# Performance work log

Hardware: AMD Instinct MI355X
Metric: run time of the kernel (lower is better)

The kernel has to match this reference:

```python
import jax, jax.numpy as jnp
import numpy as np
import math

D_MODEL = 1024
N_HEADS = 16
D_KV = 64
NUM_BUCKETS = 32
MAX_DISTANCE = 128
BATCH = 4
SEQ = 2048


def _relative_position_bucket(relative_position, num_buckets=NUM_BUCKETS, max_distance=MAX_DISTANCE):
    # bidirectional=True (encoder)
    num_buckets //= 2
    relative_buckets = (relative_position > 0).astype(jnp.int32) * num_buckets
    rp = jnp.abs(relative_position)
    max_exact = num_buckets // 2
    is_small = rp < max_exact
    rp_safe = jnp.maximum(rp, 1)  # avoid log(0); masked by is_small anyway
    rp_if_large = max_exact + (
        jnp.log(rp_safe.astype(jnp.float32) / max_exact)
        / math.log(max_distance / max_exact)
        * (num_buckets - max_exact)
    ).astype(jnp.int32)
    rp_if_large = jnp.minimum(rp_if_large, num_buckets - 1)
    relative_buckets += jnp.where(is_small, rp, rp_if_large)
    return relative_buckets


def compute_bias(rel_bias, q_len, k_len):
    context = jnp.arange(q_len)[:, None]
    memory = jnp.arange(k_len)[None, :]
    buckets = _relative_position_bucket(memory - context)  # [q, k]
    values = rel_bias[buckets]                              # [q, k, h]
    return jnp.transpose(values, (2, 0, 1))[None]           # [1, h, q, k]


def setup_inputs() -> dict:
    key = jax.random.key(0)
    ks = jax.random.split(key, 6)
    s = 1.0 / math.sqrt(D_MODEL)
    return {
        "hidden_states": jax.random.normal(ks[0], (BATCH, SEQ, D_MODEL), jnp.float32),
        "wq": jax.random.normal(ks[1], (D_MODEL, N_HEADS * D_KV), jnp.float32) * s,
        "wk": jax.random.normal(ks[2], (D_MODEL, N_HEADS * D_KV), jnp.float32) * s,
        "wv": jax.random.normal(ks[3], (D_MODEL, N_HEADS * D_KV), jnp.float32) * s,
        "wo": jax.random.normal(ks[4], (N_HEADS * D_KV, D_MODEL), jnp.float32) * s,
        "rel_bias": jax.random.normal(ks[5], (NUM_BUCKETS, N_HEADS), jnp.float32) * 0.5,
    }


def reference(hidden_states, wq, wk, wv, wo, rel_bias):
    B, S, _ = hidden_states.shape

    def shape(x):  # [B,S,H*Dk] -> [B,H,S,Dk]
        return x.reshape(B, S, N_HEADS, D_KV).transpose(0, 2, 1, 3)

    q = shape(hidden_states @ wq)
    k = shape(hidden_states @ wk)
    v = shape(hidden_states @ wv)

    # NOTE: T5 does NOT scale by 1/sqrt(d_kv)
    scores = jnp.einsum("bhqd,bhkd->bhqk", q, k)
    position_bias = compute_bias(rel_bias, S, S)  # [1,H,S,S]
    scores = scores + position_bias
    attn = jax.nn.softmax(scores.astype(jnp.float32), axis=-1).astype(scores.dtype)
    ctx = jnp.einsum("bhqk,bhkd->bhqd", attn, v)
    ctx = ctx.transpose(0, 2, 1, 3).reshape(B, S, N_HEADS * D_KV)
    return ctx @ wo
```

## Files before the change

kernel.cpp:

```cpp
#include <hip/hip_runtime.h>
#include <hip/hip_bf16.h>

typedef unsigned short u16;
typedef unsigned int   u32;
typedef __bf16 bf16x8 __attribute__((ext_vector_type(8)));
typedef float  f32x4  __attribute__((ext_vector_type(4)));
typedef u16    u16x8  __attribute__((ext_vector_type(8)));
typedef u16    u16x4  __attribute__((ext_vector_type(4)));

#define MFMA16(a,b,c) __builtin_amdgcn_mfma_f32_16x16x32_bf16(a,b,c,0,0,0)
#define LOG2E 1.4426950408889634f

__device__ __forceinline__ u16 f2b(float f) {
    u32 u = __builtin_bit_cast(u32, f);
    u32 r = (u + 0x7FFFu + ((u >> 16) & 1u)) >> 16;
    return (u16)r;
}

typedef const __attribute__((address_space(1))) u32* gaddr_t;
typedef __attribute__((address_space(3))) u32*       laddr_t;
__device__ __forceinline__ void gl_lds16(const void* g, void* l) {
    __builtin_amdgcn_global_load_lds((gaddr_t)g, (laddr_t)l, 16, 0, 0);
}

__global__ __launch_bounds__(256) void prep_kernel(
        const float* __restrict__ H, const float* __restrict__ wq,
        const float* __restrict__ wk, const float* __restrict__ wv,
        const float* __restrict__ wo, const float* __restrict__ rel_bias,
        u16* __restrict__ Hb, u16* __restrict__ Wt, u16* __restrict__ Wot,
        float* __restrict__ tab) {
    __shared__ u16 tile[64 * 72];
    int bi = blockIdx.x;
    int t = threadIdx.x;
    if (bi < 4096) {
        int i = (bi * 256 + t) * 8;
        float4 a = *(const float4*)(H + i);
        float4 b = *(const float4*)(H + i + 4);
        u16x8 o = { f2b(a.x), f2b(a.y), f2b(a.z), f2b(a.w),
                    f2b(b.x), f2b(b.y), f2b(b.z), f2b(b.w) };
        *(u16x8*)(Hb + i) = o;
    } else if (bi < 5120) {
        int g2 = bi - 4096;
        int g = g2 >> 8, rem = g2 & 255;
        int n0 = (rem >> 4) * 64, k0 = (rem & 15) * 64;
        const float* src = (g == 0) ? wq : (g == 1) ? wk : (g == 2) ? wv : wo;
        u16* dst = (g < 3) ? (Wt + g * 1048576) : Wot;
#pragma unroll
        for (int rr = 0; rr < 4; ++rr) {
            int idx = rr * 256 + t;
            int kr = idx >> 4, c = idx & 15;
            float4 v = *(const float4*)(src + (k0 + kr) * 1024 + n0 + c * 4);
            u16x4 o = { f2b(v.x), f2b(v.y), f2b(v.z), f2b(v.w) };
            *(u16x4*)&tile[kr * 72 + c * 4] = o;
        }
        __syncthreads();
#pragma unroll
        for (int rr = 0; rr < 2; ++rr) {
            int idx = rr * 256 + t;
            int n = idx >> 3, c = idx & 7;
            u16x8 o;
#pragma unroll
            for (int j = 0; j < 8; ++j) o[j] = tile[(c * 8 + j) * 72 + n];
            *(u16x8*)(dst + (n0 + n) * 1024 + k0 + c * 8) = o;
        }
    } else {
        int i = (bi - 5120) * 256 + t;
        int h = i >> 12;
        int idx = i & 4095;
        int delta = idx - 2048;
        int bucket = (delta > 0) ? 16 : 0;
        int rp = delta < 0 ? -delta : delta;
        if (rp < 8) {
            bucket += rp;
        } else {
            double v = log((double)rp / 8.0) / log(16.0) * 8.0;
            int tt = (int)v;
            int b2 = 8 + tt;
            bucket += (b2 < 15) ? b2 : 15;
        }
        tab[h * 4096 + idx] = rel_bias[bucket * 16 + h] * LOG2E;
    }
}

template <int MODE>
__global__ __launch_bounds__(256) void gemm_bt(
        const u16* __restrict__ A, const u16* __restrict__ Bt, int K, int N,
        u16* __restrict__ q_out, u16* __restrict__ k_out, u16* __restrict__ v_out,
        float* __restrict__ f_out) {
    __shared__ u16 As[128 * 32];
    __shared__ u16 Bs[128 * 32];
    __shared__ u16 vt_tile[MODE == 0 ? 128 * 136 : 1];
    int t = threadIdx.x;
    int lane = t & 63, w = t >> 6;
    int wm = w & 1, wn = w >> 1;
    int ln = lane & 15, quad = lane >> 4;
    int m0 = blockIdx.x * 128, n0 = blockIdx.y * 128;
    const u16* Ab = A + m0 * K;
    const u16* Bb = Bt + n0 * K;
    f32x4 acc[4][4] = {};
    int nk = K >> 5;
    for (int kt = 0; kt < nk; ++kt) {
        int k0 = kt * 32;
#pragma unroll
        for (int rr = 0; rr < 2; ++rr) {
            int idx = rr * 256 + t;
            int row = idx >> 2, c = (idx & 3) ^ (row & 3);
            gl_lds16(Ab + row * K + k0 + c * 8, ((char*)As) + idx * 16);
            gl_lds16(Bb + row * K + k0 + c * 8, ((char*)Bs) + idx * 16);
        }
        __syncthreads();
        bf16x8 af[4], bfr[4];
#pragma unroll
        for (int mb = 0; mb < 4; ++mb) {
            int row = wm * 64 + mb * 16 + ln;
            af[mb] = *(const bf16x8*)&As[row * 32 + ((quad ^ (row & 3)) << 3)];
        }
#pragma unroll
        for (int nb = 0; nb < 4; ++nb) {
            int row = wn * 64 + nb * 16 + ln;
            bfr[nb] = *(const bf16x8*)&Bs[row * 32 + ((quad ^ (row & 3)) << 3)];
        }
#pragma unroll
        for (int mb = 0; mb < 4; ++mb)
#pragma unroll
            for (int nb = 0; nb < 4; ++nb)
                acc[mb][nb] = MFMA16(af[mb], bfr[nb], acc[mb][nb]);
        __syncthreads();
    }
    if (MODE == 0 && n0 >= 2048) {
#pragma unroll
        for (int mb = 0; mb < 4; ++mb)
#pragma unroll
            for (int nb = 0; nb < 4; ++nb)
#pragma unroll
                for (int r = 0; r < 4; ++r) {
                    int np = wn * 64 + nb * 16 + ln;
                    int mp = wm * 64 + mb * 16 + quad * 4 + r;
                    vt_tile[np * 136 + mp] = f2b(acc[mb][nb][r]);
                }
        __syncthreads();
        int h0 = (n0 >> 6) & 15;
        int b = m0 >> 11;
        int s0 = m0 & 2047;
#pragma unroll
        for (int j = 0; j < 8; ++j) {
            int e = j * 256 + t;
            int d_all = e >> 4;
            int sc = e & 15;
            int hh = h0 + (d_all >> 6);
            int d = d_all & 63;
            u16x8 val = *(const u16x8*)&vt_tile[d_all * 136 + sc * 8];
            *(u16x8*)(v_out + (b * 16 + hh) * 131072 + d * 2048 + s0 + sc * 8) = val;
        }
    } else {
#pragma unroll
        for (int mb = 0; mb < 4; ++mb)
#pragma unroll
            for (int nb = 0; nb < 4; ++nb)
#pragma unroll
                for (int r = 0; r < 4; ++r) {
                    int m = m0 + wm * 64 + mb * 16 + quad * 4 + r;
                    int n = n0 + wn * 64 + nb * 16 + ln;
                    float v = acc[mb][nb][r];
                    if (MODE == 0) {
                        int which = n >> 10, h = (n >> 6) & 15, d = n & 63;
                        int b = m >> 11, s = m & 2047;
                        u16* dst = (which == 0) ? q_out : k_out;
                        float scale = (which == 0) ? LOG2E : 1.0f;
                        dst[(((b << 4) + h) * 2048 + s) * 64 + d] = f2b(v * scale);
                    } else {
                        f_out[m * N + n] = v;
                    }
                }
    }
}

__global__ __launch_bounds__(256, 3) void attn_kernel(
        const u16* __restrict__ Qb, const u16* __restrict__ Kb,
        const u16* __restrict__ Vt, const float* __restrict__ bias_tab,
        u16* __restrict__ ctx) {
    __shared__ u16 Ks[2][64 * 64];
    __shared__ u16 Vs[2][64 * 64];
    __shared__ u16 Ps[4][16 * 64];
    __shared__ float sb[384];
    int t = threadIdx.x;
    int lane = t & 63, w = t >> 6;
    int ln = lane & 15, quad = lane >> 4;
    int bh = blockIdx.x >> 5;
    int qtile = blockIdx.x & 31;
    int h = bh & 15, b = bh >> 4;
    int q0 = qtile * 64;

    float chi = bias_tab[h * 4096 + 2048 + 1500];
    float clo = bias_tab[h * 4096 + 2048 - 1500];

    const float* tb = bias_tab + h * 4096 + 1857;
    for (int i = t; i < 384; i += 256) sb[i] = tb[i];

    int qa = q0 + w * 16 + ln;
    const u16* qptr = Qb + (bh * 2048 + qa) * 64 + quad * 8;
    bf16x8 qf0 = *(const bf16x8*)(qptr);
    bf16x8 qf1 = *(const bf16x8*)(qptr + 32);

    const u16* Kbase = Kb + bh * 2048 * 64;
    const u16* Vbase = Vt + bh * 64 * 2048;

    f32x4 oacc[4] = {};
    float l_i = 0.0f;
    int cb2_base = 191 - w * 16 + quad * 4 - ln;
    int swl = ln & 7;

    auto stage = [&](int kb, int bufidx) {
#pragma unroll
        for (int it = 0; it < 2; ++it) {
            int idx = it * 256 + t;
            int row = idx >> 3, c = (idx & 7) ^ (row & 7);
            gl_lds16(Kbase + (kb + row) * 64 + c * 8,
                     ((char*)&Ks[bufidx][0]) + idx * 16);
            gl_lds16(Vbase + row * 2048 + kb + c * 8,
                     ((char*)&Vs[bufidx][0]) + idx * 16);
        }
    };

    auto compute = [&](int kb0, const u16* Kc, const u16* Vc) {
        f32x4 sacc[4];
        int diff = kb0 - q0;
        if (diff >= 192 || diff <= -192) {
            float c0 = (diff > 0) ? chi : clo;
            f32x4 ci = {c0, c0, c0, c0};
            __builtin_amdgcn_s_setprio(1);
#pragma unroll
            for (int nb = 0; nb < 4; ++nb) {
                int key = nb * 16 + ln;
                int sw = key & 7;
                bf16x8 kf0 = *(const bf16x8*)&Kc[key * 64 + ((quad ^ sw) << 3)];
                bf16x8 kf1 = *(const bf16x8*)&Kc[key * 64 + (((quad ^ 4) ^ sw) << 3)];
                f32x4 scc = MFMA16(kf0, qf0, ci);
                sacc[nb] = MFMA16(kf1, qf1, scc);
            }
            __builtin_amdgcn_s_setprio(0);
        } else {
            int cb = diff + cb2_base;
            __builtin_amdgcn_s_setprio(1);
#pragma unroll
            for (int nb = 0; nb < 4; ++nb) {
                int key = nb * 16 + ln;
                int sw = key & 7;
                const float* bp = &sb[cb + nb * 16];
                f32x4 ci = {bp[0], bp[1], bp[2], bp[3]};
                bf16x8 kf0 = *(const bf16x8*)&Kc[key * 64 + ((quad ^ sw) << 3)];
                bf16x8 kf1 = *(const bf16x8*)&Kc[key * 64 + (((quad ^ 4) ^ sw) << 3)];
                f32x4 scc = MFMA16(kf0, qf0, ci);
                sacc[nb] = MFMA16(kf1, qf1, scc);
            }
            __builtin_amdgcn_s_setprio(0);
        }

        float p[4][4];
        float ls0 = 0.f, ls1 = 0.f, ls2 = 0.f, ls3 = 0.f;
#pragma unroll
        for (int nb = 0; nb < 4; ++nb) {
            float e0 = __builtin_amdgcn_exp2f(sacc[nb][0]);
            float e1 = __builtin_amdgcn_exp2f(sacc[nb][1]);
            float e2 = __builtin_amdgcn_exp2f(sacc[nb][2]);
            float e3 = __builtin_amdgcn_exp2f(sacc[nb][3]);
            p[nb][0] = e0; p[nb][1] = e1; p[nb][2] = e2; p[nb][3] = e3;
            ls0 += e0; ls1 += e1; ls2 += e2; ls3 += e3;
        }
        l_i += (ls0 + ls1) + (ls2 + ls3);

        u16* pw = &Ps[w][0];
#pragma unroll
        for (int nb = 0; nb < 4; ++nb) {
            u32 lo, hi;
            asm("v_cvt_pk_bf16_f32 %0, %1, %2" : "=v"(lo) : "v"(p[nb][0]), "v"(p[nb][1]));
            asm("v_cvt_pk_bf16_f32 %0, %1, %2" : "=v"(hi) : "v"(p[nb][2]), "v"(p[nb][3]));
            int c = nb * 2 + (quad >> 1);
            u32* dst = (u32*)&pw[ln * 64 + ((c ^ swl) << 3) + (quad & 1) * 4];
            dst[0] = lo;
            dst[1] = hi;
        }

#pragma unroll
        for (int kc = 0; kc < 2; ++kc) {
            bf16x8 pf = *(const bf16x8*)&pw[ln * 64 + (((kc * 4 + quad) ^ swl) << 3)];
            __builtin_amdgcn_s_setprio(1);
#pragma unroll
            for (int nb = 0; nb < 4; ++nb) {
                int d = nb * 16 + ln;
                int vc = (kc * 4 + quad) ^ (d & 7);
                bf16x8 vf = *(const bf16x8*)&Vc[d * 64 + (vc << 3)];
                oacc[nb] = MFMA16(pf, vf, oacc[nb]);
            }
            __builtin_amdgcn_s_setprio(0);
        }
    };

    stage(0, 0);
    for (int kt = 0; kt < 31; ++kt) {
        int cur = kt & 1;
        stage((kt + 1) * 64, cur ^ 1);
        asm volatile("s_waitcnt vmcnt(4)" ::: "memory");
        __builtin_amdgcn_sched_barrier(0);
        __builtin_amdgcn_s_barrier();
        compute(kt * 64, &Ks[cur][0], &Vs[cur][0]);
        __builtin_amdgcn_s_barrier();
    }
    asm volatile("s_waitcnt vmcnt(0)" ::: "memory");
    __builtin_amdgcn_sched_barrier(0);
    __builtin_amdgcn_s_barrier();
    compute(31 * 64, &Ks[1][0], &Vs[1][0]);

    l_i += __shfl_xor(l_i, 16);
    l_i += __shfl_xor(l_i, 32);
    float linv = 1.0f / l_i;
#pragma unroll
    for (int r = 0; r < 4; ++r) {
        float lr = __shfl(linv, quad * 4 + r);
        int q = q0 + w * 16 + quad * 4 + r;
#pragma unroll
        for (int nb = 0; nb < 4; ++nb)
            ctx[(b * 2048 + q) * 1024 + h * 64 + nb * 16 + ln] = f2b(oacc[nb][r] * lr);
    }
}

extern "C" void kernel_launch(void* const* d_in, const int* in_sizes, int n_in,
                              void* d_out, int out_size, void* d_ws, size_t ws_size,
                              hipStream_t stream) {
    const float* H   = (const float*)d_in[0];
    const float* wq  = (const float*)d_in[1];
    const float* wk  = (const float*)d_in[2];
    const float* wv  = (const float*)d_in[3];
    const float* wo  = (const float*)d_in[4];
    const float* rel = (const float*)d_in[5];
    float* out = (float*)d_out;

    char* ws = (char*)d_ws;
    u16* Hb    = (u16*)(ws);
    u16* Wt    = (u16*)(ws + 16777216);
    u16* Wot   = (u16*)(ws + 23068672);
    u16* Qb    = (u16*)(ws + 25165824);
    u16* Kb    = (u16*)(ws + 41943040);
    u16* Vt    = (u16*)(ws + 58720256);
    float* bias_tab = (float*)(ws + 75497472);
    u16* ctx = Hb;

    prep_kernel<<<5376, 256, 0, stream>>>(H, wq, wk, wv, wo, rel, Hb, Wt, Wot, bias_tab);
    gemm_bt<0><<<dim3(64, 24), 256, 0, stream>>>(Hb, Wt, 1024, 3072, Qb, Kb, Vt, nullptr);
    attn_kernel<<<2048, 256, 0, stream>>>(Qb, Kb, Vt, bias_tab, ctx);
    gemm_bt<1><<<dim3(64, 8), 256, 0, stream>>>(ctx, Wot, 1024, 1024, nullptr, nullptr, nullptr, out);
}
```

Before: 307.0 us.

## Process two query tiles per attention block and keep P in registers

Each attention block now handles 128 queries (two 64-row groups) against each staged K/V tile, halving the number of blocks and the K/V global-to-LDS staging traffic per query. The P·V product is computed with 16x16x16 MFMAs and V as the A operand, so the exponentiated probabilities stay in registers instead of being written to and read back from LDS. Block-to-(head,qtile) mapping is swizzled, occupancy hint is raised to 4, and output stores are vectorized. It raises register pressure and uses the smaller-K MFMA, which issues twice as many PV instructions.

```diff
diff --git a/kernel.cpp b/kernel.cpp
--- a/kernel.cpp
+++ b/kernel.cpp
@@ -4,12 +4,28 @@
 typedef unsigned short u16;
 typedef unsigned int   u32;
 typedef __bf16 bf16x8 __attribute__((ext_vector_type(8)));
+typedef __bf16 bf16x4 __attribute__((ext_vector_type(4)));
+typedef short  s16x4  __attribute__((ext_vector_type(4)));
 typedef float  f32x4  __attribute__((ext_vector_type(4)));
 typedef u16    u16x8  __attribute__((ext_vector_type(8)));
 typedef u16    u16x4  __attribute__((ext_vector_type(4)));
+typedef u32    u32x2  __attribute__((ext_vector_type(2)));
 
 #define MFMA16(a,b,c) __builtin_amdgcn_mfma_f32_16x16x32_bf16(a,b,c,0,0,0)
 #define LOG2E 1.4426950408889634f
+
+__device__ __forceinline__ f32x4 mfma16k16(bf16x4 a, bf16x4 b, f32x4 c) {
+#if __has_builtin(__builtin_amdgcn_mfma_f32_16x16x16bf16_1k)
+    return __builtin_amdgcn_mfma_f32_16x16x16bf16_1k(
+        __builtin_bit_cast(s16x4, a), __builtin_bit_cast(s16x4, b), c, 0, 0, 0);
+#elif __has_builtin(__builtin_amdgcn_mfma_f32_16x16x16_bf16_1k)
+    return __builtin_amdgcn_mfma_f32_16x16x16_bf16_1k(
+        __builtin_bit_cast(s16x4, a), __builtin_bit_cast(s16x4, b), c, 0, 0, 0);
+#else
+    asm("v_mfma_f32_16x16x16_bf16 %0, %1, %2, %0" : "+v"(c) : "v"(a), "v"(b));
+    return c;
+#endif
+}
 
 __device__ __forceinline__ u16 f2b(float f) {
     u32 u = __builtin_bit_cast(u32, f);
@@ -175,21 +191,21 @@
     }
 }
 
-__global__ __launch_bounds__(256, 3) void attn_kernel(
+__global__ __launch_bounds__(256, 4) void attn_kernel(
         const u16* __restrict__ Qb, const u16* __restrict__ Kb,
         const u16* __restrict__ Vt, const float* __restrict__ bias_tab,
         u16* __restrict__ ctx) {
     __shared__ u16 Ks[2][64 * 64];
     __shared__ u16 Vs[2][64 * 64];
-    __shared__ u16 Ps[4][16 * 64];
     __shared__ float sb[384];
     int t = threadIdx.x;
     int lane = t & 63, w = t >> 6;
     int ln = lane & 15, quad = lane >> 4;
-    int bh = blockIdx.x >> 5;
-    int qtile = blockIdx.x & 31;
+    int bid = blockIdx.x;
+    int bh = (bid & 7) * 8 + (bid >> 7);
+    int qtile = (bid >> 3) & 15;
     int h = bh & 15, b = bh >> 4;
-    int q0 = qtile * 64;
+    int q0 = qtile * 128;
 
     float chi = bias_tab[h * 4096 + 2048 + 1500];
     float clo = bias_tab[h * 4096 + 2048 - 1500];
@@ -197,18 +213,19 @@
     const float* tb = bias_tab + h * 4096 + 1857;
     for (int i = t; i < 384; i += 256) sb[i] = tb[i];
 
-    int qa = q0 + w * 16 + ln;
-    const u16* qptr = Qb + (bh * 2048 + qa) * 64 + quad * 8;
-    bf16x8 qf0 = *(const bf16x8*)(qptr);
-    bf16x8 qf1 = *(const bf16x8*)(qptr + 32);
+    const u16* qbase = Qb + (bh * 2048 + q0 + w * 16 + ln) * 64 + quad * 8;
+    bf16x8 qf[2][2];
+    qf[0][0] = *(const bf16x8*)(qbase);
+    qf[0][1] = *(const bf16x8*)(qbase + 32);
+    qf[1][0] = *(const bf16x8*)(qbase + 64 * 64);
+    qf[1][1] = *(const bf16x8*)(qbase + 64 * 64 + 32);
 
     const u16* Kbase = Kb + bh * 2048 * 64;
     const u16* Vbase = Vt + bh * 64 * 2048;
 
-    f32x4 oacc[4] = {};
-    float l_i = 0.0f;
+    f32x4 oacc[2][4] = {};
+    float l0 = 0.0f, l1 = 0.0f;
     int cb2_base = 191 - w * 16 + quad * 4 - ln;
-    int swl = ln & 7;
 
     auto stage = [&](int kb, int bufidx) {
 #pragma unroll
@@ -223,80 +240,74 @@
     };
 
     auto compute = [&](int kb0, const u16* Kc, const u16* Vc) {
-        f32x4 sacc[4];
-        int diff = kb0 - q0;
-        if (diff >= 192 || diff <= -192) {
-            float c0 = (diff > 0) ? chi : clo;
-            f32x4 ci = {c0, c0, c0, c0};
-            __builtin_amdgcn_s_setprio(1);
+        f32x4 sacc[2][4];
+        int diffs[2] = {kb0 - q0, kb0 - q0 - 64};
+        __builtin_amdgcn_s_setprio(1);
+#pragma unroll
+        for (int nb = 0; nb < 4; ++nb) {
+            int key = nb * 16 + ln;
+            int sw = key & 7;
+            bf16x8 kf0 = *(const bf16x8*)&Kc[key * 64 + ((quad ^ sw) << 3)];
+            bf16x8 kf1 = *(const bf16x8*)&Kc[key * 64 + (((quad ^ 4) ^ sw) << 3)];
+#pragma unroll
+            for (int g = 0; g < 2; ++g) {
+                int diff = diffs[g];
+                f32x4 ci;
+                if (diff >= 192 || diff <= -192) {
+                    float c0 = (diff > 0) ? chi : clo;
+                    ci = {c0, c0, c0, c0};
+                } else {
+                    const float* bp = &sb[diff + cb2_base + nb * 16];
+                    ci = {bp[0], bp[1], bp[2], bp[3]};
+                }
+                f32x4 scc = MFMA16(kf0, qf[g][0], ci);
+                sacc[g][nb] = MFMA16(kf1, qf[g][1], scc);
+            }
+        }
+        __builtin_amdgcn_s_setprio(0);
+
+        bf16x4 pb[2][4];
+#pragma unroll
+        for (int g = 0; g < 2; ++g) {
+            float s0 = 0.f, s1 = 0.f, s2 = 0.f, s3 = 0.f;
 #pragma unroll
             for (int nb = 0; nb < 4; ++nb) {
-                int key = nb * 16 + ln;
-                int sw = key & 7;
-                bf16x8 kf0 = *(const bf16x8*)&Kc[key * 64 + ((quad ^ sw) << 3)];
-                bf16x8 kf1 = *(const bf16x8*)&Kc[key * 64 + (((quad ^ 4) ^ sw) << 3)];
-                f32x4 scc = MFMA16(kf0, qf0, ci);
-                sacc[nb] = MFMA16(kf1, qf1, scc);
+                float e0 = __builtin_amdgcn_exp2f(sacc[g][nb][0]);
+                float e1 = __builtin_amdgcn_exp2f(sacc[g][nb][1]);
+                float e2 = __builtin_amdgcn_exp2f(sacc[g][nb][2]);
+                float e3 = __builtin_amdgcn_exp2f(sacc[g][nb][3]);
+                s0 += e0; s1 += e1; s2 += e2; s3 += e3;
+                u32 lo, hi;
+                asm("v_cvt_pk_bf16_f32 %0, %1, %2" : "=v"(lo) : "v"(e0), "v"(e1));
+                asm("v_cvt_pk_bf16_f32 %0, %1, %2" : "=v"(hi) : "v"(e2), "v"(e3));
+                u32x2 uv = {lo, hi};
+                pb[g][nb] = __builtin_bit_cast(bf16x4, uv);
             }
-            __builtin_amdgcn_s_setprio(0);
-        } else {
-            int cb = diff + cb2_base;
-            __builtin_amdgcn_s_setprio(1);
-#pragma unroll
-            for (int nb = 0; nb < 4; ++nb) {
-                int key = nb * 16 + ln;
-                int sw = key & 7;
-                const float* bp = &sb[cb + nb * 16];
-                f32x4 ci = {bp[0], bp[1], bp[2], bp[3]};
-                bf16x8 kf0 = *(const bf16x8*)&Kc[key * 64 + ((quad ^ sw) << 3)];
-                bf16x8 kf1 = *(const bf16x8*)&Kc[key * 64 + (((quad ^ 4) ^ sw) << 3)];
-                f32x4 scc = MFMA16(kf0, qf0, ci);
-                sacc[nb] = MFMA16(kf1, qf1, scc);
+            if (g == 0) l0 += (s0 + s1) + (s2 + s3);
+            else        l1 += (s0 + s1) + (s2 + s3);
+        }
+
+        __builtin_amdgcn_s_setprio(1);
+#pragma unroll
+        for (int kc = 0; kc < 4; ++kc) {
+            bf16x4 vA[4];
+#pragma unroll
+            for (int nd = 0; nd < 4; ++nd) {
+                int d = nd * 16 + ln;
+                int ch = (kc * 2 + (quad >> 1)) ^ (d & 7);
+                vA[nd] = *(const bf16x4*)&Vc[d * 64 + (ch << 3) + ((quad & 1) << 2)];
             }
-            __builtin_amdgcn_s_setprio(0);
-        }
-
-        float p[4][4];
-        float ls0 = 0.f, ls1 = 0.f, ls2 = 0.f, ls3 = 0.f;
-#pragma unroll
-        for (int nb = 0; nb < 4; ++nb) {
-            float e0 = __builtin_amdgcn_exp2f(sacc[nb][0]);
-            float e1 = __builtin_amdgcn_exp2f(sacc[nb][1]);
-            float e2 = __builtin_amdgcn_exp2f(sacc[nb][2]);
-            float e3 = __builtin_amdgcn_exp2f(sacc[nb][3]);
-            p[nb][0] = e0; p[nb][1] = e1; p[nb][2] = e2; p[nb][3] = e3;
-            ls0 += e0; ls1 += e1; ls2 += e2; ls3 += e3;
-        }
-        l_i += (ls0 + ls1) + (ls2 + ls3);
-
-        u16* pw = &Ps[w][0];
-#pragma unroll
-        for (int nb = 0; nb < 4; ++nb) {
-            u32 lo, hi;
-            asm("v_cvt_pk_bf16_f32 %0, %1, %2" : "=v"(lo) : "v"(p[nb][0]), "v"(p[nb][1]));
-            asm("v_cvt_pk_bf16_f32 %0, %1, %2" : "=v"(hi) : "v"(p[nb][2]), "v"(p[nb][3]));
-            int c = nb * 2 + (quad >> 1);
-            u32* dst = (u32*)&pw[ln * 64 + ((c ^ swl) << 3) + (quad & 1) * 4];
-            dst[0] = lo;
-            dst[1] = hi;
-        }
-
-#pragma unroll
-        for (int kc = 0; kc < 2; ++kc) {
-            bf16x8 pf = *(const bf16x8*)&pw[ln * 64 + (((kc * 4 + quad) ^ swl) << 3)];
-            __builtin_amdgcn_s_setprio(1);
-#pragma unroll
-            for (int nb = 0; nb < 4; ++nb) {
-                int d = nb * 16 + ln;
-                int vc = (kc * 4 + quad) ^ (d & 7);
-                bf16x8 vf = *(const bf16x8*)&Vc[d * 64 + (vc << 3)];
-                oacc[nb] = MFMA16(pf, vf, oacc[nb]);
-            }
-            __builtin_amdgcn_s_setprio(0);
-        }
+#pragma unroll
+            for (int nd = 0; nd < 4; ++nd)
+#pragma unroll
+                for (int g = 0; g < 2; ++g)
+                    oacc[g][nd] = mfma16k16(vA[nd], pb[g][kc], oacc[g][nd]);
+        }
+        __builtin_amdgcn_s_setprio(0);
     };
 
     stage(0, 0);
+    asm volatile("s_waitcnt lgkmcnt(0)" ::: "memory");
     for (int kt = 0; kt < 31; ++kt) {
         int cur = kt & 1;
         stage((kt + 1) * 64, cur ^ 1);
@@ -311,16 +322,19 @@
     __builtin_amdgcn_s_barrier();
     compute(31 * 64, &Ks[1][0], &Vs[1][0]);
 
-    l_i += __shfl_xor(l_i, 16);
-    l_i += __shfl_xor(l_i, 32);
-    float linv = 1.0f / l_i;
-#pragma unroll
-    for (int r = 0; r < 4; ++r) {
-        float lr = __shfl(linv, quad * 4 + r);
-        int q = q0 + w * 16 + quad * 4 + r;
-#pragma unroll
-        for (int nb = 0; nb < 4; ++nb)
-            ctx[(b * 2048 + q) * 1024 + h * 64 + nb * 16 + ln] = f2b(oacc[nb][r] * lr);
+    l0 += __shfl_xor(l0, 16); l0 += __shfl_xor(l0, 32);
+    l1 += __shfl_xor(l1, 16); l1 += __shfl_xor(l1, 32);
+    float linv[2] = {1.0f / l0, 1.0f / l1};
+#pragma unroll
+    for (int g = 0; g < 2; ++g) {
+        int q = q0 + g * 64 + w * 16 + ln;
+        u16* cp = ctx + (b * 2048 + q) * 1024 + h * 64 + quad * 4;
+#pragma unroll
+        for (int nd = 0; nd < 4; ++nd) {
+            u16x4 o = { f2b(oacc[g][nd][0] * linv[g]), f2b(oacc[g][nd][1] * linv[g]),
+                        f2b(oacc[g][nd][2] * linv[g]), f2b(oacc[g][nd][3] * linv[g]) };
+            *(u16x4*)(cp + nd * 16) = o;
+        }
     }
 }
 
@@ -347,6 +361,6 @@
 
     prep_kernel<<<5376, 256, 0, stream>>>(H, wq, wk, wv, wo, rel, Hb, Wt, Wot, bias_tab);
     gemm_bt<0><<<dim3(64, 24), 256, 0, stream>>>(Hb, Wt, 1024, 3072, Qb, Kb, Vt, nullptr);
-    attn_kernel<<<2048, 256, 0, stream>>>(Qb, Kb, Vt, bias_tab, ctx);
+    attn_kernel<<<1024, 256, 0, stream>>>(Qb, Kb, Vt, bias_tab, ctx);
     gemm_bt<1><<<dim3(64, 8), 256, 0, stream>>>(ctx, Wot, 1024, 1024, nullptr, nullptr, nullptr, out);
 }
```

Result: faster. 290.8 us (-5.3%).
